# Kernel optimization log

Measured on AMD Instinct MI355X. Metric: run time of the kernel, lower is better.

Reference implementation:

```python
import jax, jax.numpy as jnp
import numpy as np

D, FH, FW = 41, 16, 44          # depth bins (arange(4,45,1)), feat H/W = 256/16, 704/16
NX, NY, NZ = 128, 128, 1        # BEV grid from grid_conf
C_CTX = 64                      # LSS context channels
EPS = 1e-5


def _frustum():
    ds = jnp.arange(4.0, 45.0, 1.0)                 # (D,)
    xs = jnp.linspace(0.0, 703.0, FW)
    ys = jnp.linspace(0.0, 255.0, FH)
    return jnp.stack([
        jnp.broadcast_to(xs[None, None, :], (D, FH, FW)),
        jnp.broadcast_to(ys[None, :, None], (D, FH, FW)),
        jnp.broadcast_to(ds[:, None, None], (D, FH, FW)),
    ], -1)                                           # (D,FH,FW,3)


def _bn(x, g, b, m, v):
    # inference-mode BatchNorm2d, x: (B,C,H,W)
    scale = g / jnp.sqrt(v + EPS)
    return x * scale[None, :, None, None] + (b - m * scale)[None, :, None, None]


def setup_inputs() -> dict:
    key = jax.random.key(0)
    ks = jax.random.split(key, 24)
    B, N = 4, 6
    imgs = jax.random.normal(ks[0], (B, N, 3, 256, 704), jnp.float32)
    eye = jnp.eye(3, dtype=jnp.float32)
    # well-conditioned camera matrices (code takes torch.inverse of these)
    rots = eye + 0.05 * jax.random.normal(ks[1], (B, N, 3, 3), jnp.float32)
    trans = 2.0 * jax.random.normal(ks[2], (B, N, 3), jnp.float32)
    K = jnp.array([[500., 0., 352.], [0., 500., 128.], [0., 0., 1.]], jnp.float32)
    kmask = jnp.array([[1., 0., 1.], [0., 1., 1.], [0., 0., 0.]], jnp.float32)
    intrins = K + 5.0 * jax.random.normal(ks[3], (B, N, 3, 3), jnp.float32) * kmask
    post_rots = eye + 0.01 * jax.random.normal(ks[4], (B, N, 3, 3), jnp.float32)
    post_trans = jax.random.normal(ks[5], (B, N, 3), jnp.float32)
    # backbone: Conv2d(3,256,16,16) + BN(256)
    conv_w = 0.02 * jax.random.normal(ks[6], (256, 3, 16, 16), jnp.float32)
    conv_b = 0.01 * jax.random.normal(ks[7], (256,), jnp.float32)
    bn1_g = 1.0 + 0.1 * jax.random.normal(ks[8], (256,), jnp.float32)
    bn1_b = 0.1 * jax.random.normal(ks[9], (256,), jnp.float32)
    bn1_m = 0.1 * jax.random.normal(ks[10], (256,), jnp.float32)
    bn1_v = jax.random.uniform(ks[11], (256,), jnp.float32, 0.5, 1.5)
    # depth_net: Conv2d(256, D+64=105, 1)
    depth_w = 0.05 * jax.random.normal(ks[12], (D + C_CTX, 256), jnp.float32)
    depth_b = 0.01 * jax.random.normal(ks[13], (D + C_CTX,), jnp.float32)
    # BEV encoder: Conv2d(128,64,3,pad=1) + BN(64)
    enc_w = 0.05 * jax.random.normal(ks[14], (64, 128, 3, 3), jnp.float32)
    enc_b = 0.01 * jax.random.normal(ks[15], (64,), jnp.float32)
    bn2_g = 1.0 + 0.1 * jax.random.normal(ks[16], (64,), jnp.float32)
    bn2_b = 0.1 * jax.random.normal(ks[17], (64,), jnp.float32)
    bn2_m = 0.1 * jax.random.normal(ks[18], (64,), jnp.float32)
    bn2_v = jax.random.uniform(ks[19], (64,), jnp.float32, 0.5, 1.5)
    # head: Conv2d(64, 7, 1)
    head_w = 0.05 * jax.random.normal(ks[20], (7, 64), jnp.float32)
    head_b = 0.01 * jax.random.normal(ks[21], (7,), jnp.float32)
    return dict(curr_imgs=imgs, rots=rots, trans=trans, intrins=intrins,
                post_rots=post_rots, post_trans=post_trans,
                conv_w=conv_w, conv_b=conv_b, bn1_g=bn1_g, bn1_b=bn1_b,
                bn1_m=bn1_m, bn1_v=bn1_v, depth_w=depth_w, depth_b=depth_b,
                enc_w=enc_w, enc_b=enc_b, bn2_g=bn2_g, bn2_b=bn2_b,
                bn2_m=bn2_m, bn2_v=bn2_v, head_w=head_w, head_b=head_b)


def _forward(curr_imgs, rots, trans, intrins, post_rots, post_trans,
             conv_w, conv_b, bn1_g, bn1_b, bn1_m, bn1_v,
             depth_w, depth_b, enc_w, enc_b, bn2_g, bn2_b, bn2_m, bn2_v,
             head_w, head_b):
    B, N = curr_imgs.shape[:2]
    dn = ('NCHW', 'OIHW', 'NCHW')
    # backbone (patchify conv + BN + ReLU)
    x = curr_imgs.reshape(B * N, 3, 256, 704)
    x = jax.lax.conv_general_dilated(x, conv_w, (16, 16), 'VALID', dimension_numbers=dn)
    x = jax.nn.relu(_bn(x + conv_b[None, :, None, None], bn1_g, bn1_b, bn1_m, bn1_v))  # (BN,256,16,44)
    # depth net (1x1 conv) -> depth softmax + context
    y = jnp.einsum('oc,bchw->bohw', depth_w, x) + depth_b[None, :, None, None]
    depth = jax.nn.softmax(y[:, :D], axis=1)                 # (BN,D,H,W)
    ctx = y[:, D:]                                           # (BN,C,H,W)
    # LSS outer product: (BN,C,D,H,W) -> (B,N,D,H,W,C)
    outer = ctx[:, :, None] * depth[:, None]
    outer = outer.reshape(B, N, C_CTX, D, FH, FW).transpose(0, 1, 3, 4, 5, 2)
    # geometry: pixel frustum -> ego coords
    fr = _frustum()                                          # (D,FH,FW,3)
    pts = fr[None, None] - post_trans[:, :, None, None, None, :]
    pts = jnp.einsum('bnij,bndhwj->bndhwi', jnp.linalg.inv(post_rots), pts)
    pts = jnp.concatenate([pts[..., :2] * pts[..., 2:3], pts[..., 2:3]], -1)
    comb = rots @ jnp.linalg.inv(intrins)
    pts = jnp.einsum('bnij,bndhwj->bndhwi', comb, pts) + trans[:, :, None, None, None, :]
    # voxel pooling (segment-sum == sort+cumsum trick of the original)
    dx = jnp.array([0.8, 0.8, 20.0], jnp.float32)
    low = jnp.array([-51.2, -51.2, -10.0], jnp.float32)      # bx - dx/2
    coords = ((pts.reshape(-1, 3) - low) / dx).astype(jnp.int32)  # trunc-to-zero like .long()
    rank = coords[:, 0] + coords[:, 1] * NX + coords[:, 2] * NX * NY
    tot = NX * NY * NZ
    kept = (rank >= 0) & (rank < tot)                        # combined-rank check only (as in source)
    feats = outer.reshape(-1, C_CTX) * kept[:, None].astype(outer.dtype)
    bev_flat = jax.ops.segment_sum(feats, jnp.where(kept, rank, 0), num_segments=tot)
    bev = bev_flat.reshape(NZ, NY, NX, C_CTX).transpose(0, 3, 1, 2)  # (1,64,128,128); batch mixed as in source
    # temporal fusion (prev_bev=None branch): cat(bev, bev)
    feat = jnp.concatenate([bev, bev], 1)                    # (1,128,128,128)
    feat = jax.lax.conv_general_dilated(feat, enc_w, (1, 1), 'SAME', dimension_numbers=dn)
    feat = jax.nn.relu(_bn(feat + enc_b[None, :, None, None], bn2_g, bn2_b, bn2_m, bn2_v))
    out = jnp.einsum('oc,bchw->bohw', head_w, feat) + head_b[None, :, None, None]
    return out, bev


def reference(curr_imgs, rots, trans, intrins, post_rots, post_trans,
              conv_w, conv_b, bn1_g, bn1_b, bn1_m, bn1_v,
              depth_w, depth_b, enc_w, enc_b, bn2_g, bn2_b, bn2_m, bn2_v,
              head_w, head_b):
    return _forward(curr_imgs, rots, trans, intrins, post_rots, post_trans,
                    conv_w, conv_b, bn1_g, bn1_b, bn1_m, bn1_v,
                    depth_w, depth_b, enc_w, enc_b, bn2_g, bn2_b, bn2_m, bn2_v,
                    head_w, head_b)
```

## Files before the change

### kernel.cpp

```cpp
#include <hip/hip_runtime.h>
#include <hip/hip_bf16.h>
#include <hip/hip_fp16.h>

#define NPTS 692736
#define NPATCH 16896

typedef _Float16 h16;
typedef __attribute__((ext_vector_type(4))) _Float16 half4v;
typedef __attribute__((ext_vector_type(8))) _Float16 half8v;
typedef __attribute__((ext_vector_type(4))) float f32x4;

__device__ float  v11_xbuf[NPATCH*256];
__device__ float  v11_ctx[NPATCH*64];
__device__ float  v11_depth[NPATCH*41];
__device__ int    v11_ranks[NPTS];
__device__ float  v11_bev[16384*64];
__device__ double v11_geom[24*24];

__device__ h16    v14_whi[256*768];
__device__ h16    v14_wlo[256*768];

__device__ h16    v15_dwhi[112*256];
__device__ h16    v15_dwlo[112*256];

__device__ h16    v16_w2hi[64*576];
__device__ h16    v16_w2lo[64*576];

__device__ int    v12_cnt[16384];
__device__ int    v12_off[16384];
__device__ int    v12_pos[NPTS];
__device__ int2   v12_sorted[NPTS];
__device__ int    v12_total;

__device__ __forceinline__ void inv3_v11(const double* m, double* o){
  double a=m[0],b=m[1],c=m[2],d=m[3],e=m[4],f=m[5],g=m[6],h=m[7],i=m[8];
  double A = e*i - f*h, B = -(d*i - f*g), C = d*h - e*g;
  double det = a*A + b*B + c*C;
  double id = 1.0/det;
  o[0]=A*id;            o[1]=-(b*i - c*h)*id; o[2]=(b*f - c*e)*id;
  o[3]=B*id;            o[4]=(a*i - c*g)*id;  o[5]=-(a*f - c*d)*id;
  o[6]=C*id;            o[7]=-(a*h - b*g)*id; o[8]=(a*e - b*d)*id;
}

__global__ void zero_v13(){
  int gid = blockIdx.x*256 + threadIdx.x;
  v11_bev[gid] = 0.f;
  if (gid < 16384) v12_cnt[gid] = 0;
}

__global__ void geom_v11(const float* rots, const float* trans, const float* intrins,
                         const float* post_rots, const float* post_trans){
  int t = threadIdx.x;
  if (t >= 24) return;
  double pr[9], it[9], r[9];
  for (int i=0;i<9;i++){
    pr[i] = (double)post_rots[t*9+i];
    it[i] = (double)intrins[t*9+i];
    r[i]  = (double)rots[t*9+i];
  }
  double ipr[9], iit[9];
  inv3_v11(pr, ipr); inv3_v11(it, iit);
  double* g = v11_geom + t*24;
  for (int i=0;i<3;i++) for(int j=0;j<3;j++){
    double s=0; for(int k=0;k<3;k++) s += r[i*3+k]*iit[k*3+j];
    g[9+i*3+j]=s;
  }
  for (int i=0;i<9;i++) g[i]   = ipr[i];
  for (int i=0;i<3;i++) g[18+i]= (double)post_trans[t*3+i];
  for (int i=0;i<3;i++) g[21+i]= (double)trans[t*3+i];
}

__global__ void wt_v14(const float* cw){
  int gid = blockIdx.x*256 + threadIdx.x;
  float x = cw[gid];
  h16 hi = (h16)x;
  h16 lo = (h16)(x - (float)hi);
  v14_whi[gid] = hi;
  v14_wlo[gid] = lo;
}

__global__ void wtd_v15(const float* dw){
  int gid = blockIdx.x*256 + threadIdx.x;
  int o = gid >> 8, c = gid & 255;
  float x = (o < 105) ? dw[o*256 + c] : 0.f;
  h16 hi = (h16)x;
  h16 lo = (h16)(x - (float)hi);
  v15_dwhi[gid] = hi;
  v15_dwlo[gid] = lo;
}

__global__ void w2_v16(const float* enc_w){
  int gid = blockIdx.x*256 + threadIdx.x;
  if (gid >= 36864) return;
  int o = gid / 576; int k = gid % 576;
  int tap = k >> 6, ic = k & 63;
  float x = enc_w[o*1152 + ic*9 + tap] + enc_w[o*1152 + (ic+64)*9 + tap];
  h16 hi = (h16)x;
  h16 lo = (h16)(x - (float)hi);
  v16_w2hi[gid] = hi;
  v16_w2lo[gid] = lo;
}

__global__ __launch_bounds__(256) void conv1_v14(const float* img,
    const float* cb, const float* g1, const float* b1, const float* m1, const float* v1){
  __shared__ h16 Ah[64*40];
  __shared__ h16 Al[64*40];
  __shared__ h16 Bh[128*40];
  __shared__ h16 Bl[128*40];
  int tid  = threadIdx.x;
  int lane = tid & 63, wv = tid >> 6;
  int wr = wv >> 1, wc = wv & 1;
  int pbase = blockIdx.x * 64;
  int obase = blockIdx.y * 128;

  const float* abase[2];
  int app[2], akq[2];
  #pragma unroll
  for (int i=0;i<2;i++){
    int l = tid + i*256;
    int pp = l>>3; int kq4 = (l&7)*4;
    app[i] = pp; akq[i] = kq4;
    int p = pbase + pp;
    int im = p/704; int pix = p%704;
    int ph = pix/44, pw = pix%44;
    abase[i] = img + (size_t)im*540672 + (size_t)ph*16*704 + pw*16;
  }
  const h16* wsh[4]; const h16* wsl[4];
  int wo[4], wkq[4];
  #pragma unroll
  for (int i=0;i<4;i++){
    int l = tid + i*256;
    int o = l>>3; int kq4 = (l&7)*4;
    wo[i] = o; wkq[i] = kq4;
    wsh[i] = v14_whi + (size_t)(obase+o)*768 + kq4;
    wsl[i] = v14_wlo + (size_t)(obase+o)*768 + kq4;
  }

  f32x4 acc[2][4];
  #pragma unroll
  for (int mf=0;mf<2;mf++)
    #pragma unroll
    for (int nf=0;nf<4;nf++) acc[mf][nf] = (f32x4){0.f,0.f,0.f,0.f};

  int fr = lane & 15, fg = lane >> 4;
  int koff = fg*8;

  for (int kt=0; kt<768; kt+=32){
    __syncthreads();
    #pragma unroll
    for (int i=0;i<2;i++){
      int k0 = kt + akq[i];
      int c = k0>>8, rem = k0&255, ky = rem>>4, kx = rem&15;
      float4 v = *(const float4*)(abase[i] + (size_t)c*180224 + ky*704 + kx);
      half4v hv, lv;
      hv.x = (h16)v.x; lv.x = (h16)(v.x - (float)hv.x);
      hv.y = (h16)v.y; lv.y = (h16)(v.y - (float)hv.y);
      hv.z = (h16)v.z; lv.z = (h16)(v.z - (float)hv.z);
      hv.w = (h16)v.w; lv.w = (h16)(v.w - (float)hv.w);
      *(half4v*)&Ah[app[i]*40 + akq[i]] = hv;
      *(half4v*)&Al[app[i]*40 + akq[i]] = lv;
    }
    #pragma unroll
    for (int i=0;i<4;i++){
      half4v hv = *(const half4v*)(wsh[i] + kt);
      half4v lv = *(const half4v*)(wsl[i] + kt);
      *(half4v*)&Bh[wo[i]*40 + wkq[i]] = hv;
      *(half4v*)&Bl[wo[i]*40 + wkq[i]] = lv;
    }
    __syncthreads();
    half8v ah[2], al[2], bh[4], bl[4];
    #pragma unroll
    for (int mf=0;mf<2;mf++){
      int row = wr*32 + mf*16 + fr;
      ah[mf] = *(const half8v*)&Ah[row*40 + koff];
      al[mf] = *(const half8v*)&Al[row*40 + koff];
    }
    #pragma unroll
    for (int nf=0;nf<4;nf++){
      int col = wc*64 + nf*16 + fr;
      bh[nf] = *(const half8v*)&Bh[col*40 + koff];
      bl[nf] = *(const half8v*)&Bl[col*40 + koff];
    }
    #pragma unroll
    for (int mf=0;mf<2;mf++)
      #pragma unroll
      for (int nf=0;nf<4;nf++){
        acc[mf][nf] = __builtin_amdgcn_mfma_f32_16x16x32_f16(ah[mf], bh[nf], acc[mf][nf], 0,0,0);
        acc[mf][nf] = __builtin_amdgcn_mfma_f32_16x16x32_f16(ah[mf], bl[nf], acc[mf][nf], 0,0,0);
        acc[mf][nf] = __builtin_amdgcn_mfma_f32_16x16x32_f16(al[mf], bh[nf], acc[mf][nf], 0,0,0);
      }
  }
  #pragma unroll
  for (int nf=0;nf<4;nf++){
    int ch = obase + wc*64 + nf*16 + fr;
    float sc = g1[ch] / sqrtf(v1[ch] + 1e-5f);
    float sh = b1[ch] - m1[ch]*sc;
    float bi = cb[ch];
    #pragma unroll
    for (int mf=0;mf<2;mf++){
      #pragma unroll
      for (int j=0;j<4;j++){
        int p = pbase + wr*32 + mf*16 + fg*4 + j;
        float t = (acc[mf][nf][j] + bi)*sc + sh;
        v11_xbuf[(size_t)p*256 + ch] = t > 0.f ? t : 0.f;
      }
    }
  }
}

__global__ __launch_bounds__(256) void depth_v15(const float* db){
  __shared__ h16 Ah[64*40];
  __shared__ h16 Al[64*40];
  __shared__ h16 Bh[112*40];
  __shared__ h16 Bl[112*40];
  __shared__ float sy[64*113];
  int tid = threadIdx.x;
  int lane = tid & 63, wv = tid >> 6;
  int pbase = blockIdx.x*64;
  int fr = lane & 15, fg = lane >> 4;
  int koff = fg*8;

  f32x4 acc[7];
  #pragma unroll
  for (int nf=0;nf<7;nf++) acc[nf] = (f32x4){0.f,0.f,0.f,0.f};

  for (int kt=0; kt<256; kt+=32){
    __syncthreads();
    #pragma unroll
    for (int i=0;i<2;i++){
      int l = tid + i*256;
      int pp = l>>3, kq4 = (l&7)*4;
      float4 v = *(const float4*)&v11_xbuf[(size_t)(pbase+pp)*256 + kt + kq4];
      half4v hv, lv;
      hv.x = (h16)v.x; lv.x = (h16)(v.x - (float)hv.x);
      hv.y = (h16)v.y; lv.y = (h16)(v.y - (float)hv.y);
      hv.z = (h16)v.z; lv.z = (h16)(v.z - (float)hv.z);
      hv.w = (h16)v.w; lv.w = (h16)(v.w - (float)hv.w);
      *(half4v*)&Ah[pp*40 + kq4] = hv;
      *(half4v*)&Al[pp*40 + kq4] = lv;
    }
    #pragma unroll
    for (int i=0;i<4;i++){
      int l = tid + i*256;
      if (l < 896){
        int o = l>>3, kq4 = (l&7)*4;
        *(half4v*)&Bh[o*40 + kq4] = *(const half4v*)&v15_dwhi[o*256 + kt + kq4];
        *(half4v*)&Bl[o*40 + kq4] = *(const half4v*)&v15_dwlo[o*256 + kt + kq4];
      }
    }
    __syncthreads();
    int row = wv*16 + fr;
    half8v ah = *(const half8v*)&Ah[row*40 + koff];
    half8v al = *(const half8v*)&Al[row*40 + koff];
    #pragma unroll
    for (int nf=0;nf<7;nf++){
      int col = nf*16 + fr;
      half8v bh = *(const half8v*)&Bh[col*40 + koff];
      half8v bl = *(const half8v*)&Bl[col*40 + koff];
      acc[nf] = __builtin_amdgcn_mfma_f32_16x16x32_f16(ah, bh, acc[nf], 0,0,0);
      acc[nf] = __builtin_amdgcn_mfma_f32_16x16x32_f16(ah, bl, acc[nf], 0,0,0);
      acc[nf] = __builtin_amdgcn_mfma_f32_16x16x32_f16(al, bh, acc[nf], 0,0,0);
    }
  }
  #pragma unroll
  for (int nf=0;nf<7;nf++){
    int o = nf*16 + fr;
    if (o < 105){
      float bias = db[o];
      #pragma unroll
      for (int j=0;j<4;j++){
        int pp = wv*16 + fg*4 + j;
        sy[pp*113 + o] = acc[nf][j] + bias;
      }
    }
  }
  __syncthreads();
  if (tid < 64){
    float* y = &sy[tid*113];
    float m = y[0];
    for (int i=1;i<41;i++) m = fmaxf(m, y[i]);
    float s = 0.f;
    for (int i=0;i<41;i++){ float e = expf(y[i]-m); y[i] = e; s += e; }
    float inv = 1.f/s;
    for (int i=0;i<41;i++) y[i] *= inv;
  }
  __syncthreads();
  for (int l = tid; l < 64*41; l += 256){
    int pp = l/41, dd = l%41;
    v11_depth[(size_t)(pbase+pp)*41 + dd] = sy[pp*113+dd];
  }
  for (int l = tid; l < 64*64; l += 256){
    int pp = l>>6, c = l&63;
    v11_ctx[(size_t)(pbase+pp)*64 + c] = sy[pp*113 + 41 + c];
  }
}

__global__ __launch_bounds__(256) void rank_v13(){
  __shared__ int lh[16384];
  int tid = threadIdx.x;
  for (int i = tid; i < 16384; i += 256) lh[i] = 0;
  __syncthreads();
  int base = blockIdx.x*1024;
  int rk[4], lp[4];
  #pragma unroll
  for (int k=0;k<4;k++){
    int idx = base + k*256 + tid;
    rk[k] = -1; lp[k] = 0;
    if (idx < NPTS){
      int im = idx / 28864;
      int r  = idx % 28864;
      int d  = r / 704; int pix = r % 704;
      int h = pix / 44, w = pix % 44;
      const double* g = v11_geom + im*24;
      double fx = (double)w * (703.0/43.0);
      double fy = (double)h * 17.0;
      double fz = 4.0 + (double)d;
      double px = fx - g[18], py = fy - g[19], pz = fz - g[20];
      double q0 = g[0]*px + g[1]*py + g[2]*pz;
      double q1 = g[3]*px + g[4]*py + g[5]*pz;
      double q2 = g[6]*px + g[7]*py + g[8]*pz;
      q0 *= q2; q1 *= q2;
      double o0 = g[9]*q0  + g[10]*q1 + g[11]*q2 + g[21];
      double o1 = g[12]*q0 + g[13]*q1 + g[14]*q2 + g[22];
      double o2 = g[15]*q0 + g[16]*q1 + g[17]*q2 + g[23];
      int cx = (int)((o0 + 51.2)/0.8);
      int cy = (int)((o1 + 51.2)/0.8);
      int cz = (int)((o2 + 10.0)/20.0);
      int rank = cx + cy*128 + cz*16384;
      if (rank >= 0 && rank < 16384){
        rk[k] = rank;
        lp[k] = atomicAdd(&lh[rank], 1);
      }
    }
  }
  __syncthreads();
  for (int i = tid; i < 16384; i += 256){
    int h = lh[i];
    if (h) lh[i] = atomicAdd(&v12_cnt[i], h);
  }
  __syncthreads();
  #pragma unroll
  for (int k=0;k<4;k++){
    int idx = base + k*256 + tid;
    if (idx < NPTS){
      v11_ranks[idx] = rk[k];
      if (rk[k] >= 0) v12_pos[idx] = lh[rk[k]] + lp[k];
    }
  }
}

__global__ __launch_bounds__(256) void scan_v13(){
  __shared__ int part[256];
  int t = threadIdx.x;
  int base = t*64;
  int s = 0;
  for (int i=0;i<64;i++) s += v12_cnt[base+i];
  part[t] = s;
  __syncthreads();
  if (t == 0){
    int run = 0;
    for (int i=0;i<256;i++){ int v = part[i]; part[i] = run; run += v; }
    v12_total = run;
  }
  __syncthreads();
  int run = part[t];
  for (int i=0;i<64;i++){
    v12_off[base+i] = run;
    run += v12_cnt[base+i];
  }
}

__global__ __launch_bounds__(256) void fill_v13(){
  int idx = blockIdx.x*256 + threadIdx.x;
  if (idx >= NPTS) return;
  int rank = v11_ranks[idx];
  if (rank < 0) return;
  int im = idx / 28864;
  int r  = idx % 28864;
  int d  = r / 704; int pix = r % 704;
  int p  = im*704 + pix;
  int pos = v12_off[rank] + v12_pos[idx];
  v12_sorted[pos] = make_int2((p<<6) | d, rank);
}

__global__ __launch_bounds__(256) void gather_v13(){
  int total = v12_total;
  int w = threadIdx.x >> 6;
  int chunk = blockIdx.x*256 + w*64;
  if (chunk >= total) return;
  int lane = threadIdx.x & 63;
  int n = total - chunk; if (n > 64) n = 64;
  int pv = 0, rv = -1;
  float dv = 0.f;
  if (lane < n){
    int2 sr = v12_sorted[chunk + lane];
    pv = sr.x; rv = sr.y;
    dv = v11_depth[(pv>>6)*41 + (pv & 63)];
  }
  float acc = 0.f;
  int cur = __shfl(rv, 0);
  for (int i = 0; i < n; i++){
    int rk = __shfl(rv, i);
    int pp = __shfl(pv, i) >> 6;
    float dd = __shfl(dv, i);
    if (rk != cur){
      atomicAdd(&v11_bev[(size_t)cur*64 + lane], acc);
      acc = 0.f; cur = rk;
    }
    acc += v11_ctx[(pp<<6) | lane] * dd;
  }
  atomicAdd(&v11_bev[(size_t)cur*64 + lane], acc);
}

__global__ void bevout_v11(float* out1){
  int gid = blockIdx.x*256 + threadIdx.x;
  int c  = gid >> 14;
  int yx = gid & 16383;
  out1[gid] = v11_bev[(size_t)yx*64 + c];
}

__global__ __launch_bounds__(256) void conv2_v16(
    const float* eb, const float* g2, const float* b2_, const float* m2, const float* v2,
    const float* hw, const float* hb, float* out0){
  __shared__ h16 Ah[64*40];
  __shared__ h16 Al[64*40];
  __shared__ h16 Bh[64*40];
  __shared__ h16 Bl[64*40];
  __shared__ float sfeat[64*68];
  __shared__ float hred[4*64*7];
  int tid = threadIdx.x;
  int lane = tid & 63, wv = tid >> 6;
  int bx = blockIdx.x & 15, by = blockIdx.x >> 4;
  int fr = lane & 15, fg = lane >> 4;
  int koff = fg*8;

  f32x4 acc[4];
  #pragma unroll
  for (int nf=0;nf<4;nf++) acc[nf] = (f32x4){0.f,0.f,0.f,0.f};

  for (int kt=0; kt<576; kt+=32){
    int tap = kt >> 6, ic0 = kt & 32;
    int dy = tap/3 - 1, dx = tap%3 - 1;
    __syncthreads();
    #pragma unroll
    for (int i=0;i<2;i++){
      int l = tid + i*256;
      int pp = l>>3, q4 = (l&7)*4;
      int py = pp>>3, px = pp&7;
      int gy = by*8 + py + dy, gx = bx*8 + px + dx;
      float4 v = {0.f,0.f,0.f,0.f};
      if (gy>=0 && gy<128 && gx>=0 && gx<128)
        v = *(const float4*)&v11_bev[(size_t)(gy*128+gx)*64 + ic0 + q4];
      half4v hv, lv;
      hv.x = (h16)v.x; lv.x = (h16)(v.x - (float)hv.x);
      hv.y = (h16)v.y; lv.y = (h16)(v.y - (float)hv.y);
      hv.z = (h16)v.z; lv.z = (h16)(v.z - (float)hv.z);
      hv.w = (h16)v.w; lv.w = (h16)(v.w - (float)hv.w);
      *(half4v*)&Ah[pp*40 + q4] = hv;
      *(half4v*)&Al[pp*40 + q4] = lv;
    }
    #pragma unroll
    for (int i=0;i<2;i++){
      int l = tid + i*256;
      int o = l>>3, q4 = (l&7)*4;
      *(half4v*)&Bh[o*40 + q4] = *(const half4v*)&v16_w2hi[o*576 + kt + q4];
      *(half4v*)&Bl[o*40 + q4] = *(const half4v*)&v16_w2lo[o*576 + kt + q4];
    }
    __syncthreads();
    int row = wv*16 + fr;
    half8v ah = *(const half8v*)&Ah[row*40 + koff];
    half8v al = *(const half8v*)&Al[row*40 + koff];
    #pragma unroll
    for (int nf=0;nf<4;nf++){
      int col = nf*16 + fr;
      half8v bh = *(const half8v*)&Bh[col*40 + koff];
      half8v bl = *(const half8v*)&Bl[col*40 + koff];
      acc[nf] = __builtin_amdgcn_mfma_f32_16x16x32_f16(ah, bh, acc[nf], 0,0,0);
      acc[nf] = __builtin_amdgcn_mfma_f32_16x16x32_f16(ah, bl, acc[nf], 0,0,0);
      acc[nf] = __builtin_amdgcn_mfma_f32_16x16x32_f16(al, bh, acc[nf], 0,0,0);
    }
  }
  #pragma unroll
  for (int nf=0;nf<4;nf++){
    int ch = nf*16 + fr;
    float sc = g2[ch]/sqrtf(v2[ch]+1e-5f);
    float sh = b2_[ch] - m2[ch]*sc;
    float bi = eb[ch];
    #pragma unroll
    for (int j=0;j<4;j++){
      int pp = wv*16 + fg*4 + j;
      float t = (acc[nf][j] + bi)*sc + sh;
      sfeat[pp*68 + ch] = t > 0.f ? t : 0.f;
    }
  }
  __syncthreads();
  int og = tid >> 6, pix = tid & 63;
  float part[7];
  #pragma unroll
  for (int o=0;o<7;o++) part[o]=0.f;
  #pragma unroll
  for (int j=0;j<16;j++){
    int oc = og*16 + j;
    float v = sfeat[pix*68 + oc];
    #pragma unroll
    for (int o=0;o<7;o++) part[o] += hw[o*64+oc]*v;
  }
  #pragma unroll
  for (int o=0;o<7;o++) hred[(og*64+pix)*7+o] = part[o];
  __syncthreads();
  if (og == 0){
    int gy = by*8 + (pix>>3), gx = bx*8 + (pix&7);
    #pragma unroll
    for (int o=0;o<7;o++){
      float s = hred[pix*7+o] + hred[(64+pix)*7+o] + hred[(128+pix)*7+o]
              + hred[(192+pix)*7+o] + hb[o];
      out0[o*16384 + gy*128 + gx] = s;
    }
  }
}

extern "C" void kernel_launch(void* const* d_in, const int* in_sizes, int n_in,
                              void* d_out, int out_size, void* d_ws, size_t ws_size,
                              hipStream_t stream){
  const float* imgs       = (const float*)d_in[0];
  const float* rots       = (const float*)d_in[1];
  const float* trans      = (const float*)d_in[2];
  const float* intrins    = (const float*)d_in[3];
  const float* post_rots  = (const float*)d_in[4];
  const float* post_trans = (const float*)d_in[5];
  const float* conv_w     = (const float*)d_in[6];
  const float* conv_b     = (const float*)d_in[7];
  const float* bn1_g      = (const float*)d_in[8];
  const float* bn1_b      = (const float*)d_in[9];
  const float* bn1_m      = (const float*)d_in[10];
  const float* bn1_v      = (const float*)d_in[11];
  const float* depth_w    = (const float*)d_in[12];
  const float* depth_b    = (const float*)d_in[13];
  const float* enc_w      = (const float*)d_in[14];
  const float* enc_b      = (const float*)d_in[15];
  const float* bn2_g      = (const float*)d_in[16];
  const float* bn2_b      = (const float*)d_in[17];
  const float* bn2_m      = (const float*)d_in[18];
  const float* bn2_v      = (const float*)d_in[19];
  const float* head_w     = (const float*)d_in[20];
  const float* head_b     = (const float*)d_in[21];

  float* out0 = (float*)d_out;
  float* out1 = out0 + 114688;

  zero_v13<<<4096, 256, 0, stream>>>();
  geom_v11<<<1, 32, 0, stream>>>(rots, trans, intrins, post_rots, post_trans);
  wt_v14<<<768, 256, 0, stream>>>(conv_w);
  wtd_v15<<<112, 256, 0, stream>>>(depth_w);
  w2_v16<<<144, 256, 0, stream>>>(enc_w);
  conv1_v14<<<dim3(264, 2), 256, 0, stream>>>(imgs, conv_b, bn1_g, bn1_b, bn1_m, bn1_v);
  depth_v15<<<264, 256, 0, stream>>>(depth_b);
  rank_v13<<<(NPTS+1023)/1024, 256, 0, stream>>>();
  scan_v13<<<1, 256, 0, stream>>>();
  fill_v13<<<NPTS/256, 256, 0, stream>>>();
  gather_v13<<<NPTS/256, 256, 0, stream>>>();
  bevout_v11<<<4096, 256, 0, stream>>>(out1);
  conv2_v16<<<256, 256, 0, stream>>>(enc_b, bn2_g, bn2_b, bn2_m, bn2_v,
                                     head_w, head_b, out0);
}
```

Before: 286.3 us.

## Use k-chunk-major LDS layout with 8-wide loads in MFMA GEMM kernels

Reorganizes the shared-memory tiles of conv1, depth and conv2 from padded row-major (stride 40) to a [kchunk][row][8] layout, so each thread stages 8 contiguous halves with 128-bit loads and stores. Fragment reads become contiguous 16-byte rows, which is meant to reduce LDS bank conflicts and the number of staging instructions. conv1 also doubles its K step to 64 per barrier, halving the number of synchronizations at the cost of more LDS.

```diff
diff --git a/kernel.cpp b/kernel.cpp
--- a/kernel.cpp
+++ b/kernel.cpp
@@ -101,40 +101,31 @@
   v16_w2lo[gid] = lo;
 }
 
-__global__ __launch_bounds__(256) void conv1_v14(const float* img,
+__global__ __launch_bounds__(256) void conv1_v17(const float* img,
     const float* cb, const float* g1, const float* b1, const float* m1, const float* v1){
-  __shared__ h16 Ah[64*40];
-  __shared__ h16 Al[64*40];
-  __shared__ h16 Bh[128*40];
-  __shared__ h16 Bl[128*40];
+  __shared__ __align__(16) h16 Ah[8][64][8];
+  __shared__ __align__(16) h16 Al[8][64][8];
+  __shared__ __align__(16) h16 Bh[8][128][8];
+  __shared__ __align__(16) h16 Bl[8][128][8];
   int tid  = threadIdx.x;
   int lane = tid & 63, wv = tid >> 6;
   int wr = wv >> 1, wc = wv & 1;
   int pbase = blockIdx.x * 64;
   int obase = blockIdx.y * 128;
 
-  const float* abase[2];
-  int app[2], akq[2];
-  #pragma unroll
-  for (int i=0;i<2;i++){
-    int l = tid + i*256;
-    int pp = l>>3; int kq4 = (l&7)*4;
-    app[i] = pp; akq[i] = kq4;
-    int p = pbase + pp;
-    int im = p/704; int pix = p%704;
-    int ph = pix/44, pw = pix%44;
-    abase[i] = img + (size_t)im*540672 + (size_t)ph*16*704 + pw*16;
-  }
-  const h16* wsh[4]; const h16* wsl[4];
-  int wo[4], wkq[4];
-  #pragma unroll
-  for (int i=0;i<4;i++){
-    int l = tid + i*256;
-    int o = l>>3; int kq4 = (l&7)*4;
-    wo[i] = o; wkq[i] = kq4;
-    wsh[i] = v14_whi + (size_t)(obase+o)*768 + kq4;
-    wsl[i] = v14_wlo + (size_t)(obase+o)*768 + kq4;
-  }
+  int app = tid & 63;
+  {
+  }
+  int p = pbase + app;
+  int im = p/704, pix = p%704;
+  int ph = pix/44, pw = pix%44;
+  const float* abase = img + (size_t)im*540672 + (size_t)ph*16*704 + pw*16;
+  int kcA0 = tid >> 6;
+
+  int bo = tid & 127;
+  const h16* wbh = v14_whi + (size_t)(obase+bo)*768;
+  const h16* wbl = v14_wlo + (size_t)(obase+bo)*768;
+  int kcB0 = tid >> 7;
 
   f32x4 acc[2][4];
   #pragma unroll
@@ -143,52 +134,56 @@
     for (int nf=0;nf<4;nf++) acc[mf][nf] = (f32x4){0.f,0.f,0.f,0.f};
 
   int fr = lane & 15, fg = lane >> 4;
-  int koff = fg*8;
-
-  for (int kt=0; kt<768; kt+=32){
+
+  for (int kt=0; kt<768; kt+=64){
     __syncthreads();
     #pragma unroll
     for (int i=0;i<2;i++){
-      int k0 = kt + akq[i];
+      int kc = kcA0 + 4*i;
+      int k0 = kt + kc*8;
       int c = k0>>8, rem = k0&255, ky = rem>>4, kx = rem&15;
-      float4 v = *(const float4*)(abase[i] + (size_t)c*180224 + ky*704 + kx);
-      half4v hv, lv;
-      hv.x = (h16)v.x; lv.x = (h16)(v.x - (float)hv.x);
-      hv.y = (h16)v.y; lv.y = (h16)(v.y - (float)hv.y);
-      hv.z = (h16)v.z; lv.z = (h16)(v.z - (float)hv.z);
-      hv.w = (h16)v.w; lv.w = (h16)(v.w - (float)hv.w);
-      *(half4v*)&Ah[app[i]*40 + akq[i]] = hv;
-      *(half4v*)&Al[app[i]*40 + akq[i]] = lv;
+      const float* src = abase + (size_t)c*180224 + ky*704 + kx;
+      float4 v0 = *(const float4*)src;
+      float4 v1 = *(const float4*)(src+4);
+      float vv[8] = {v0.x,v0.y,v0.z,v0.w,v1.x,v1.y,v1.z,v1.w};
+      half8v hv, lv;
+      #pragma unroll
+      for (int e=0;e<8;e++){ h16 h=(h16)vv[e]; hv[e]=h; lv[e]=(h16)(vv[e]-(float)h); }
+      *(half8v*)&Ah[kc][app][0] = hv;
+      *(half8v*)&Al[kc][app][0] = lv;
     }
     #pragma unroll
     for (int i=0;i<4;i++){
-      half4v hv = *(const half4v*)(wsh[i] + kt);
-      half4v lv = *(const half4v*)(wsl[i] + kt);
-      *(half4v*)&Bh[wo[i]*40 + wkq[i]] = hv;
-      *(half4v*)&Bl[wo[i]*40 + wkq[i]] = lv;
+      int kc = kcB0 + 2*i;
+      *(half8v*)&Bh[kc][bo][0] = *(const half8v*)(wbh + kt + kc*8);
+      *(half8v*)&Bl[kc][bo][0] = *(const half8v*)(wbl + kt + kc*8);
     }
     __syncthreads();
-    half8v ah[2], al[2], bh[4], bl[4];
-    #pragma unroll
-    for (int mf=0;mf<2;mf++){
-      int row = wr*32 + mf*16 + fr;
-      ah[mf] = *(const half8v*)&Ah[row*40 + koff];
-      al[mf] = *(const half8v*)&Al[row*40 + koff];
-    }
-    #pragma unroll
-    for (int nf=0;nf<4;nf++){
-      int col = wc*64 + nf*16 + fr;
-      bh[nf] = *(const half8v*)&Bh[col*40 + koff];
-      bl[nf] = *(const half8v*)&Bl[col*40 + koff];
-    }
-    #pragma unroll
-    for (int mf=0;mf<2;mf++)
+    #pragma unroll
+    for (int ks=0;ks<2;ks++){
+      int kc = ks*4 + fg;
+      half8v ah[2], al[2], bh[4], bl[4];
+      #pragma unroll
+      for (int mf=0;mf<2;mf++){
+        int row = wr*32 + mf*16 + fr;
+        ah[mf] = *(const half8v*)&Ah[kc][row][0];
+        al[mf] = *(const half8v*)&Al[kc][row][0];
+      }
       #pragma unroll
       for (int nf=0;nf<4;nf++){
-        acc[mf][nf] = __builtin_amdgcn_mfma_f32_16x16x32_f16(ah[mf], bh[nf], acc[mf][nf], 0,0,0);
-        acc[mf][nf] = __builtin_amdgcn_mfma_f32_16x16x32_f16(ah[mf], bl[nf], acc[mf][nf], 0,0,0);
-        acc[mf][nf] = __builtin_amdgcn_mfma_f32_16x16x32_f16(al[mf], bh[nf], acc[mf][nf], 0,0,0);
+        int col = wc*64 + nf*16 + fr;
+        bh[nf] = *(const half8v*)&Bh[kc][col][0];
+        bl[nf] = *(const half8v*)&Bl[kc][col][0];
       }
+      #pragma unroll
+      for (int mf=0;mf<2;mf++)
+        #pragma unroll
+        for (int nf=0;nf<4;nf++){
+          acc[mf][nf] = __builtin_amdgcn_mfma_f32_16x16x32_f16(ah[mf], bh[nf], acc[mf][nf], 0,0,0);
+          acc[mf][nf] = __builtin_amdgcn_mfma_f32_16x16x32_f16(ah[mf], bl[nf], acc[mf][nf], 0,0,0);
+          acc[mf][nf] = __builtin_amdgcn_mfma_f32_16x16x32_f16(al[mf], bh[nf], acc[mf][nf], 0,0,0);
+        }
+    }
   }
   #pragma unroll
   for (int nf=0;nf<4;nf++){
@@ -200,25 +195,28 @@
     for (int mf=0;mf<2;mf++){
       #pragma unroll
       for (int j=0;j<4;j++){
-        int p = pbase + wr*32 + mf*16 + fg*4 + j;
+        int pq = pbase + wr*32 + mf*16 + fg*4 + j;
         float t = (acc[mf][nf][j] + bi)*sc + sh;
-        v11_xbuf[(size_t)p*256 + ch] = t > 0.f ? t : 0.f;
+        v11_xbuf[(size_t)pq*256 + ch] = t > 0.f ? t : 0.f;
       }
     }
   }
 }
 
-__global__ __launch_bounds__(256) void depth_v15(const float* db){
-  __shared__ h16 Ah[64*40];
-  __shared__ h16 Al[64*40];
-  __shared__ h16 Bh[112*40];
-  __shared__ h16 Bl[112*40];
+__global__ __launch_bounds__(256) void depth_v16(const float* db){
+  __shared__ __align__(16) h16 Ah[4][64][8];
+  __shared__ __align__(16) h16 Al[4][64][8];
+  __shared__ __align__(16) h16 Bh[4][112][8];
+  __shared__ __align__(16) h16 Bl[4][112][8];
   __shared__ float sy[64*113];
   int tid = threadIdx.x;
   int lane = tid & 63, wv = tid >> 6;
   int pbase = blockIdx.x*64;
   int fr = lane & 15, fg = lane >> 4;
-  int koff = fg*8;
+
+  int app = tid & 63;
+  int kcA = tid >> 6;
+  const float* xsrc = &v11_xbuf[(size_t)(pbase+app)*256 + kcA*8];
 
   f32x4 acc[7];
   #pragma unroll
@@ -226,37 +224,30 @@
 
   for (int kt=0; kt<256; kt+=32){
     __syncthreads();
-    #pragma unroll
-    for (int i=0;i<2;i++){
-      int l = tid + i*256;
-      int pp = l>>3, kq4 = (l&7)*4;
-      float4 v = *(const float4*)&v11_xbuf[(size_t)(pbase+pp)*256 + kt + kq4];
-      half4v hv, lv;
-      hv.x = (h16)v.x; lv.x = (h16)(v.x - (float)hv.x);
-      hv.y = (h16)v.y; lv.y = (h16)(v.y - (float)hv.y);
-      hv.z = (h16)v.z; lv.z = (h16)(v.z - (float)hv.z);
-      hv.w = (h16)v.w; lv.w = (h16)(v.w - (float)hv.w);
-      *(half4v*)&Ah[pp*40 + kq4] = hv;
-      *(half4v*)&Al[pp*40 + kq4] = lv;
-    }
-    #pragma unroll
-    for (int i=0;i<4;i++){
-      int l = tid + i*256;
-      if (l < 896){
-        int o = l>>3, kq4 = (l&7)*4;
-        *(half4v*)&Bh[o*40 + kq4] = *(const half4v*)&v15_dwhi[o*256 + kt + kq4];
-        *(half4v*)&Bl[o*40 + kq4] = *(const half4v*)&v15_dwlo[o*256 + kt + kq4];
-      }
+    {
+      float4 v0 = *(const float4*)(xsrc + kt);
+      float4 v1 = *(const float4*)(xsrc + kt + 4);
+      float vv[8] = {v0.x,v0.y,v0.z,v0.w,v1.x,v1.y,v1.z,v1.w};
+      half8v hv, lv;
+      #pragma unroll
+      for (int e=0;e<8;e++){ h16 h=(h16)vv[e]; hv[e]=h; lv[e]=(h16)(vv[e]-(float)h); }
+      *(half8v*)&Ah[kcA][app][0] = hv;
+      *(half8v*)&Al[kcA][app][0] = lv;
+    }
+    for (int l = tid; l < 448; l += 256){
+      int kc = l/112, o = l%112;
+      *(half8v*)&Bh[kc][o][0] = *(const half8v*)&v15_dwhi[o*256 + kt + kc*8];
+      *(half8v*)&Bl[kc][o][0] = *(const half8v*)&v15_dwlo[o*256 + kt + kc*8];
     }
     __syncthreads();
     int row = wv*16 + fr;
-    half8v ah = *(const half8v*)&Ah[row*40 + koff];
-    half8v al = *(const half8v*)&Al[row*40 + koff];
+    half8v ah = *(const half8v*)&Ah[fg][row][0];
+    half8v al = *(const half8v*)&Al[fg][row][0];
     #pragma unroll
     for (int nf=0;nf<7;nf++){
       int col = nf*16 + fr;
-      half8v bh = *(const half8v*)&Bh[col*40 + koff];
-      half8v bl = *(const half8v*)&Bl[col*40 + koff];
+      half8v bh = *(const half8v*)&Bh[fg][col][0];
+      half8v bl = *(const half8v*)&Bl[fg][col][0];
       acc[nf] = __builtin_amdgcn_mfma_f32_16x16x32_f16(ah, bh, acc[nf], 0,0,0);
       acc[nf] = __builtin_amdgcn_mfma_f32_16x16x32_f16(ah, bl, acc[nf], 0,0,0);
       acc[nf] = __builtin_amdgcn_mfma_f32_16x16x32_f16(al, bh, acc[nf], 0,0,0);
@@ -419,20 +410,23 @@
   out1[gid] = v11_bev[(size_t)yx*64 + c];
 }
 
-__global__ __launch_bounds__(256) void conv2_v16(
+__global__ __launch_bounds__(256) void conv2_v17(
     const float* eb, const float* g2, const float* b2_, const float* m2, const float* v2,
     const float* hw, const float* hb, float* out0){
-  __shared__ h16 Ah[64*40];
-  __shared__ h16 Al[64*40];
-  __shared__ h16 Bh[64*40];
-  __shared__ h16 Bl[64*40];
+  __shared__ __align__(16) h16 Ah[4][64][8];
+  __shared__ __align__(16) h16 Al[4][64][8];
+  __shared__ __align__(16) h16 Bh[4][64][8];
+  __shared__ __align__(16) h16 Bl[4][64][8];
   __shared__ float sfeat[64*68];
   __shared__ float hred[4*64*7];
   int tid = threadIdx.x;
   int lane = tid & 63, wv = tid >> 6;
   int bx = blockIdx.x & 15, by = blockIdx.x >> 4;
   int fr = lane & 15, fg = lane >> 4;
-  int koff = fg*8;
+
+  int app = tid & 63;
+  int kcT = tid >> 6;
+  int apy = app >> 3, apx = app & 7;
 
   f32x4 acc[4];
   #pragma unroll
@@ -442,39 +436,34 @@
     int tap = kt >> 6, ic0 = kt & 32;
     int dy = tap/3 - 1, dx = tap%3 - 1;
     __syncthreads();
-    #pragma unroll
-    for (int i=0;i<2;i++){
-      int l = tid + i*256;
-      int pp = l>>3, q4 = (l&7)*4;
-      int py = pp>>3, px = pp&7;
-      int gy = by*8 + py + dy, gx = bx*8 + px + dx;
-      float4 v = {0.f,0.f,0.f,0.f};
-      if (gy>=0 && gy<128 && gx>=0 && gx<128)
-        v = *(const float4*)&v11_bev[(size_t)(gy*128+gx)*64 + ic0 + q4];
-      half4v hv, lv;
-      hv.x = (h16)v.x; lv.x = (h16)(v.x - (float)hv.x);
-      hv.y = (h16)v.y; lv.y = (h16)(v.y - (float)hv.y);
-      hv.z = (h16)v.z; lv.z = (h16)(v.z - (float)hv.z);
-      hv.w = (h16)v.w; lv.w = (h16)(v.w - (float)hv.w);
-      *(half4v*)&Ah[pp*40 + q4] = hv;
-      *(half4v*)&Al[pp*40 + q4] = lv;
-    }
-    #pragma unroll
-    for (int i=0;i<2;i++){
-      int l = tid + i*256;
-      int o = l>>3, q4 = (l&7)*4;
-      *(half4v*)&Bh[o*40 + q4] = *(const half4v*)&v16_w2hi[o*576 + kt + q4];
-      *(half4v*)&Bl[o*40 + q4] = *(const half4v*)&v16_w2lo[o*576 + kt + q4];
+    {
+      int gy = by*8 + apy + dy, gx = bx*8 + apx + dx;
+      float4 v0 = {0.f,0.f,0.f,0.f}, v1 = {0.f,0.f,0.f,0.f};
+      if (gy>=0 && gy<128 && gx>=0 && gx<128){
+        const float* src = &v11_bev[(size_t)(gy*128+gx)*64 + ic0 + kcT*8];
+        v0 = *(const float4*)src;
+        v1 = *(const float4*)(src+4);
+      }
+      float vv[8] = {v0.x,v0.y,v0.z,v0.w,v1.x,v1.y,v1.z,v1.w};
+      half8v hv, lv;
+      #pragma unroll
+      for (int e=0;e<8;e++){ h16 h=(h16)vv[e]; hv[e]=h; lv[e]=(h16)(vv[e]-(float)h); }
+      *(half8v*)&Ah[kcT][app][0] = hv;
+      *(half8v*)&Al[kcT][app][0] = lv;
+    }
+    {
+      *(half8v*)&Bh[kcT][app][0] = *(const half8v*)&v16_w2hi[app*576 + kt + kcT*8];
+      *(half8v*)&Bl[kcT][app][0] = *(const half8v*)&v16_w2lo[app*576 + kt + kcT*8];
     }
     __syncthreads();
     int row = wv*16 + fr;
-    half8v ah = *(const half8v*)&Ah[row*40 + koff];
-    half8v al = *(const half8v*)&Al[row*40 + koff];
+    half8v ah = *(const half8v*)&Ah[fg][row][0];
+    half8v al = *(const half8v*)&Al[fg][row][0];
     #pragma unroll
     for (int nf=0;nf<4;nf++){
       int col = nf*16 + fr;
-      half8v bh = *(const half8v*)&Bh[col*40 + koff];
-      half8v bl = *(const half8v*)&Bl[col*40 + koff];
+      half8v bh = *(const half8v*)&Bh[fg][col][0];
+      half8v bl = *(const half8v*)&Bl[fg][col][0];
       acc[nf] = __builtin_amdgcn_mfma_f32_16x16x32_f16(ah, bh, acc[nf], 0,0,0);
       acc[nf] = __builtin_amdgcn_mfma_f32_16x16x32_f16(ah, bl, acc[nf], 0,0,0);
       acc[nf] = __builtin_amdgcn_mfma_f32_16x16x32_f16(al, bh, acc[nf], 0,0,0);
@@ -553,13 +542,13 @@
   wt_v14<<<768, 256, 0, stream>>>(conv_w);
   wtd_v15<<<112, 256, 0, stream>>>(depth_w);
   w2_v16<<<144, 256, 0, stream>>>(enc_w);
-  conv1_v14<<<dim3(264, 2), 256, 0, stream>>>(imgs, conv_b, bn1_g, bn1_b, bn1_m, bn1_v);
-  depth_v15<<<264, 256, 0, stream>>>(depth_b);
+  conv1_v17<<<dim3(264, 2), 256, 0, stream>>>(imgs, conv_b, bn1_g, bn1_b, bn1_m, bn1_v);
+  depth_v16<<<264, 256, 0, stream>>>(depth_b);
   rank_v13<<<(NPTS+1023)/1024, 256, 0, stream>>>();
   scan_v13<<<1, 256, 0, stream>>>();
   fill_v13<<<NPTS/256, 256, 0, stream>>>();
   gather_v13<<<NPTS/256, 256, 0, stream>>>();
   bevout_v11<<<4096, 256, 0, stream>>>(out1);
-  conv2_v16<<<256, 256, 0, stream>>>(enc_b, bn2_g, bn2_b, bn2_m, bn2_v,
+  conv2_v17<<<256, 256, 0, stream>>>(enc_b, bn2_g, bn2_b, bn2_m, bn2_v,
                                      head_w, head_b, out0);
 }
```

Measured after the change: 297.8 us. 1.04x slower.
